# Performance work log

Measured on AMD Instinct MI355X. Metric: run time of the kernel, lower is better.

Reference implementation:

```python
import jax, jax.numpy as jnp
import numpy as np

B, S, D = 8, 2048, 256


def setup_inputs() -> dict:
    key = jax.random.key(0)
    kq, kk, kv, km = jax.random.split(key, 4)
    q = jax.random.normal(kq, (B, S, D), dtype=jnp.float32)
    k = jax.random.normal(kk, (B, S, D), dtype=jnp.float32)
    v = jax.random.normal(kv, (B, S, D), dtype=jnp.float32)
    mask = jax.random.randint(km, (B, S, S), 0, 2, dtype=jnp.int32)
    return {"q": q, "k": k, "v": v, "mask": mask}


def reference(q, k, v, mask):
    d_k = q.shape[-1]
    scale = 1.0 / jnp.sqrt(jnp.float32(d_k))
    # scores: [B, S, S]
    attn = jnp.einsum('bqd,bkd->bqk', q, k) * scale
    attn = jnp.where(mask == 0, jnp.float32(-1e9), attn)
    attn = jax.nn.softmax(attn, axis=-1)
    out = jnp.einsum('bqk,bkd->bqd', attn, v)
    return (out, attn)
```

## Files before the change

kernel.cpp:

```cpp
#include <hip/hip_runtime.h>

constexpr int B = 8, S = 2048, D = 256;
constexpr int TQ = 32;
constexpr float SCALE = 0.0625f;
constexpr int PSTRIDE = 2056;

typedef __attribute__((ext_vector_type(8))) short bf16x8;
typedef __attribute__((ext_vector_type(4))) float f32x4;

__device__ __forceinline__ short f2bf(float f) {
    union { float f; unsigned u; } c; c.f = f;
    unsigned u = c.u + 0x7fffu + ((c.u >> 16) & 1u);
    return (short)(u >> 16);
}

__global__ void conv_bf16(const float* __restrict__ in, short* __restrict__ out, int n4) {
    int i = blockIdx.x * blockDim.x + threadIdx.x;
    if (i < n4) {
        float4 v = ((const float4*)in)[i];
        short4 o; o.x = f2bf(v.x); o.y = f2bf(v.y); o.z = f2bf(v.z); o.w = f2bf(v.w);
        ((short4*)out)[i] = o;
    }
}

__global__ void transpose_v(const float* __restrict__ v, short* __restrict__ vt) {
    const int b = blockIdx.z;
    const int d0 = blockIdx.x * 64, k0 = blockIdx.y * 64;
    const int t = threadIdx.x;
    const int tr = t >> 4, tc = t & 15;
    __shared__ float tile[64][65];
    const float* vb = v + (size_t)b * S * D;
    #pragma unroll
    for (int r = 0; r < 4; ++r) {
        int key = r * 16 + tr;
        float4 x = *(const float4*)(vb + (size_t)(k0 + key) * D + d0 + tc * 4);
        tile[key][tc * 4 + 0] = x.x; tile[key][tc * 4 + 1] = x.y;
        tile[key][tc * 4 + 2] = x.z; tile[key][tc * 4 + 3] = x.w;
    }
    __syncthreads();
    short* vtb = vt + (size_t)b * D * S;
    #pragma unroll
    for (int r = 0; r < 4; ++r) {
        int d = r * 16 + tr;
        short4 o;
        o.x = f2bf(tile[tc * 4 + 0][d]); o.y = f2bf(tile[tc * 4 + 1][d]);
        o.z = f2bf(tile[tc * 4 + 2][d]); o.w = f2bf(tile[tc * 4 + 3][d]);
        *(short4*)(vtb + (size_t)(d0 + d) * S + k0 + tc * 4) = o;
    }
}

__global__ __launch_bounds__(512, 2) void attn_mfma(
    const short* __restrict__ qb, const short* __restrict__ kb,
    const short* __restrict__ vtb, const int* __restrict__ maskg,
    float* __restrict__ outg, float* __restrict__ attng)
{
    const int b = blockIdx.y;
    const int i0 = blockIdx.x * TQ;
    const int tid = threadIdx.x;
    const int wave = tid >> 6, lane = tid & 63;
    const int quad = lane >> 4, l16 = lane & 15;

    __shared__ short p_lds[TQ][PSTRIDE];
    __shared__ float red[8][TQ];

    bf16x8 aq[2][8];
    const short* qbase = qb + ((size_t)b * S + i0) * D;
    #pragma unroll
    for (int mt = 0; mt < 2; ++mt)
        #pragma unroll
        for (int ks = 0; ks < 8; ++ks)
            aq[mt][ks] = *(const bf16x8*)(qbase + (size_t)(mt * 16 + l16) * D + ks * 32 + quad * 8);

    f32x4 acc[2][16];
    #pragma unroll
    for (int mt = 0; mt < 2; ++mt)
        #pragma unroll
        for (int nt = 0; nt < 16; ++nt)
            acc[mt][nt] = f32x4{0.f, 0.f, 0.f, 0.f};

    const short* kbase = kb + (size_t)b * S * D;
    #pragma unroll
    for (int nt = 0; nt < 16; ++nt) {
        const int n0 = wave * 256 + nt * 16;
        bf16x8 bk[8];
        #pragma unroll
        for (int ks = 0; ks < 8; ++ks)
            bk[ks] = *(const bf16x8*)(kbase + (size_t)(n0 + l16) * D + ks * 32 + quad * 8);
        #pragma unroll
        for (int ks = 0; ks < 8; ++ks) {
            acc[0][nt] = __builtin_amdgcn_mfma_f32_16x16x32_bf16(aq[0][ks], bk[ks], acc[0][nt], 0, 0, 0);
            acc[1][nt] = __builtin_amdgcn_mfma_f32_16x16x32_bf16(aq[1][ks], bk[ks], acc[1][nt], 0, 0, 0);
        }
    }

    float rsum[2][4];
    #pragma unroll
    for (int mt = 0; mt < 2; ++mt)
        #pragma unroll
        for (int r = 0; r < 4; ++r) rsum[mt][r] = 0.f;

    #pragma unroll
    for (int mt = 0; mt < 2; ++mt) {
        const int* mbase = maskg + ((size_t)b * S + i0 + mt * 16 + quad * 4) * S;
        #pragma unroll
        for (int nt = 0; nt < 16; ++nt) {
            const int col = wave * 256 + nt * 16 + l16;
            #pragma unroll
            for (int r = 0; r < 4; ++r) {
                int m = mbase[(size_t)r * S + col];
                float s = (m == 0) ? -1e9f : acc[mt][nt][r] * SCALE;
                float e = __expf(s);
                acc[mt][nt][r] = e;
                rsum[mt][r] += e;
            }
        }
    }
    #pragma unroll
    for (int mt = 0; mt < 2; ++mt)
        #pragma unroll
        for (int r = 0; r < 4; ++r) {
            float v = rsum[mt][r];
            v += __shfl_xor(v, 1); v += __shfl_xor(v, 2);
            v += __shfl_xor(v, 4); v += __shfl_xor(v, 8);
            rsum[mt][r] = v;
            if (l16 == 0) red[wave][mt * 16 + quad * 4 + r] = v;
        }
    __syncthreads();

    float inv[2][4];
    #pragma unroll
    for (int mt = 0; mt < 2; ++mt)
        #pragma unroll
        for (int r = 0; r < 4; ++r) {
            float tot = 0.f;
            #pragma unroll
            for (int w = 0; w < 8; ++w) tot += red[w][mt * 16 + quad * 4 + r];
            inv[mt][r] = 1.0f / tot;
        }

    #pragma unroll
    for (int mt = 0; mt < 2; ++mt) {
        float* abase = attng + ((size_t)b * S + i0 + mt * 16 + quad * 4) * S;
        #pragma unroll
        for (int nt = 0; nt < 16; ++nt) {
            const int col = wave * 256 + nt * 16 + l16;
            #pragma unroll
            for (int r = 0; r < 4; ++r) {
                float p = acc[mt][nt][r] * inv[mt][r];
                abase[(size_t)r * S + col] = p;
                p_lds[mt * 16 + quad * 4 + r][col] = f2bf(p);
            }
        }
    }
    __syncthreads();

    f32x4 oacc[2][2];
    #pragma unroll
    for (int mt = 0; mt < 2; ++mt)
        #pragma unroll
        for (int nc = 0; nc < 2; ++nc) oacc[mt][nc] = f32x4{0.f, 0.f, 0.f, 0.f};

    const short* vbase = vtb + (size_t)b * D * S;
    const int nb = wave * 32;
    for (int ks = 0; ks < 64; ++ks) {
        bf16x8 ap[2], bv[2];
        #pragma unroll
        for (int mt = 0; mt < 2; ++mt)
            ap[mt] = *(const bf16x8*)&p_lds[mt * 16 + l16][ks * 32 + quad * 8];
        #pragma unroll
        for (int nc = 0; nc < 2; ++nc)
            bv[nc] = *(const bf16x8*)(vbase + (size_t)(nb + nc * 16 + l16) * S + ks * 32 + quad * 8);
        #pragma unroll
        for (int mt = 0; mt < 2; ++mt)
            #pragma unroll
            for (int nc = 0; nc < 2; ++nc)
                oacc[mt][nc] = __builtin_amdgcn_mfma_f32_16x16x32_bf16(ap[mt], bv[nc], oacc[mt][nc], 0, 0, 0);
    }

    #pragma unroll
    for (int mt = 0; mt < 2; ++mt)
        #pragma unroll
        for (int nc = 0; nc < 2; ++nc)
            #pragma unroll
            for (int r = 0; r < 4; ++r) {
                int row = i0 + mt * 16 + quad * 4 + r;
                int col = nb + nc * 16 + l16;
                outg[((size_t)b * S + row) * D + col] = oacc[mt][nc][r];
            }
}

extern "C" void kernel_launch(void* const* d_in, const int* in_sizes, int n_in,
                              void* d_out, int out_size, void* d_ws, size_t ws_size,
                              hipStream_t stream) {
    const float* q    = (const float*)d_in[0];
    const float* k    = (const float*)d_in[1];
    const float* v    = (const float*)d_in[2];
    const int*   mask = (const int*)d_in[3];
    float* out  = (float*)d_out;
    float* attn = out + (size_t)B * S * D;

    const size_t N = (size_t)B * S * D;
    short* qb  = (short*)d_ws;
    short* kb  = qb + N;
    short* vtb = kb + N;

    const int n4 = (int)(N / 4);
    conv_bf16<<<dim3(n4 / 256), 256, 0, stream>>>(q, qb, n4);
    conv_bf16<<<dim3(n4 / 256), 256, 0, stream>>>(k, kb, n4);
    transpose_v<<<dim3(D / 64, S / 64, B), 256, 0, stream>>>(v, vtb);

    attn_mfma<<<dim3(S / TQ, B), 512, 0, stream>>>(qb, kb, vtb, mask, out, attn);
}
```

Measured before the change: 412.2 us.

## Halve query tile to 16 rows for higher occupancy, use nontemporal mask/attn loads/stores

```diff
diff --git a/kernel.cpp b/kernel.cpp
--- a/kernel.cpp
+++ b/kernel.cpp
@@ -1,7 +1,7 @@
 #include <hip/hip_runtime.h>
 
 constexpr int B = 8, S = 2048, D = 256;
-constexpr int TQ = 32;
+constexpr int TQ = 16;
 constexpr float SCALE = 0.0625f;
 constexpr int PSTRIDE = 2056;
 
@@ -49,7 +49,7 @@
     }
 }
 
-__global__ __launch_bounds__(512, 2) void attn_mfma(
+__global__ __launch_bounds__(512, 4) void attn_mfma(
     const short* __restrict__ qb, const short* __restrict__ kb,
     const short* __restrict__ vtb, const int* __restrict__ maskg,
     float* __restrict__ outg, float* __restrict__ attng)
@@ -63,20 +63,16 @@
     __shared__ short p_lds[TQ][PSTRIDE];
     __shared__ float red[8][TQ];
 
-    bf16x8 aq[2][8];
+    bf16x8 aq[8];
     const short* qbase = qb + ((size_t)b * S + i0) * D;
     #pragma unroll
-    for (int mt = 0; mt < 2; ++mt)
-        #pragma unroll
-        for (int ks = 0; ks < 8; ++ks)
-            aq[mt][ks] = *(const bf16x8*)(qbase + (size_t)(mt * 16 + l16) * D + ks * 32 + quad * 8);
+    for (int ks = 0; ks < 8; ++ks)
+        aq[ks] = *(const bf16x8*)(qbase + (size_t)l16 * D + ks * 32 + quad * 8);
 
-    f32x4 acc[2][16];
+    f32x4 acc[16];
     #pragma unroll
-    for (int mt = 0; mt < 2; ++mt)
-        #pragma unroll
-        for (int nt = 0; nt < 16; ++nt)
-            acc[mt][nt] = f32x4{0.f, 0.f, 0.f, 0.f};
+    for (int nt = 0; nt < 16; ++nt)
+        acc[nt] = f32x4{0.f, 0.f, 0.f, 0.f};
 
     const short* kbase = kb + (size_t)b * S * D;
     #pragma unroll
@@ -87,106 +83,88 @@
         for (int ks = 0; ks < 8; ++ks)
             bk[ks] = *(const bf16x8*)(kbase + (size_t)(n0 + l16) * D + ks * 32 + quad * 8);
         #pragma unroll
-        for (int ks = 0; ks < 8; ++ks) {
-            acc[0][nt] = __builtin_amdgcn_mfma_f32_16x16x32_bf16(aq[0][ks], bk[ks], acc[0][nt], 0, 0, 0);
-            acc[1][nt] = __builtin_amdgcn_mfma_f32_16x16x32_bf16(aq[1][ks], bk[ks], acc[1][nt], 0, 0, 0);
-        }
+        for (int ks = 0; ks < 8; ++ks)
+            acc[nt] = __builtin_amdgcn_mfma_f32_16x16x32_bf16(aq[ks], bk[ks], acc[nt], 0, 0, 0);
     }
 
-    float rsum[2][4];
+    float rsum[4];
     #pragma unroll
-    for (int mt = 0; mt < 2; ++mt)
-        #pragma unroll
-        for (int r = 0; r < 4; ++r) rsum[mt][r] = 0.f;
+    for (int r = 0; r < 4; ++r) rsum[r] = 0.f;
 
-    #pragma unroll
-    for (int mt = 0; mt < 2; ++mt) {
-        const int* mbase = maskg + ((size_t)b * S + i0 + mt * 16 + quad * 4) * S;
+    {
+        const int* mbase = maskg + ((size_t)b * S + i0 + quad * 4) * S;
         #pragma unroll
         for (int nt = 0; nt < 16; ++nt) {
             const int col = wave * 256 + nt * 16 + l16;
             #pragma unroll
             for (int r = 0; r < 4; ++r) {
-                int m = mbase[(size_t)r * S + col];
-                float s = (m == 0) ? -1e9f : acc[mt][nt][r] * SCALE;
+                int m = __builtin_nontemporal_load(mbase + (size_t)r * S + col);
+                float s = (m == 0) ? -1e9f : acc[nt][r] * SCALE;
                 float e = __expf(s);
-                acc[mt][nt][r] = e;
-                rsum[mt][r] += e;
+                acc[nt][r] = e;
+                rsum[r] += e;
             }
         }
     }
     #pragma unroll
-    for (int mt = 0; mt < 2; ++mt)
-        #pragma unroll
-        for (int r = 0; r < 4; ++r) {
-            float v = rsum[mt][r];
-            v += __shfl_xor(v, 1); v += __shfl_xor(v, 2);
-            v += __shfl_xor(v, 4); v += __shfl_xor(v, 8);
-            rsum[mt][r] = v;
-            if (l16 == 0) red[wave][mt * 16 + quad * 4 + r] = v;
-        }
+    for (int r = 0; r < 4; ++r) {
+        float v = rsum[r];
+        v += __shfl_xor(v, 1); v += __shfl_xor(v, 2);
+        v += __shfl_xor(v, 4); v += __shfl_xor(v, 8);
+        rsum[r] = v;
+        if (l16 == 0) red[wave][quad * 4 + r] = v;
+    }
     __syncthreads();
 
-    float inv[2][4];
+    float inv[4];
     #pragma unroll
-    for (int mt = 0; mt < 2; ++mt)
+    for (int r = 0; r < 4; ++r) {
+        float tot = 0.f;
         #pragma unroll
-        for (int r = 0; r < 4; ++r) {
-            float tot = 0.f;
-            #pragma unroll
-            for (int w = 0; w < 8; ++w) tot += red[w][mt * 16 + quad * 4 + r];
-            inv[mt][r] = 1.0f / tot;
-        }
+        for (int w = 0; w < 8; ++w) tot += red[w][quad * 4 + r];
+        inv[r] = 1.0f / tot;
+    }
 
-    #pragma unroll
-    for (int mt = 0; mt < 2; ++mt) {
-        float* abase = attng + ((size_t)b * S + i0 + mt * 16 + quad * 4) * S;
+    {
+        float* abase = attng + ((size_t)b * S + i0 + quad * 4) * S;
         #pragma unroll
         for (int nt = 0; nt < 16; ++nt) {
             const int col = wave * 256 + nt * 16 + l16;
             #pragma unroll
             for (int r = 0; r < 4; ++r) {
-                float p = acc[mt][nt][r] * inv[mt][r];
-                abase[(size_t)r * S + col] = p;
-                p_lds[mt * 16 + quad * 4 + r][col] = f2bf(p);
+                float p = acc[nt][r] * inv[r];
+                __builtin_nontemporal_store(p, abase + (size_t)r * S + col);
+                p_lds[quad * 4 + r][col] = f2bf(p);
             }
         }
     }
     __syncthreads();
 
-    f32x4 oacc[2][2];
+    f32x4 oacc[2];
     #pragma unroll
-    for (int mt = 0; mt < 2; ++mt)
-        #pragma unroll
-        for (int nc = 0; nc < 2; ++nc) oacc[mt][nc] = f32x4{0.f, 0.f, 0.f, 0.f};
+    for (int nc = 0; nc < 2; ++nc) oacc[nc] = f32x4{0.f, 0.f, 0.f, 0.f};
 
     const short* vbase = vtb + (size_t)b * D * S;
     const int nb = wave * 32;
     for (int ks = 0; ks < 64; ++ks) {
-        bf16x8 ap[2], bv[2];
-        #pragma unroll
-        for (int mt = 0; mt < 2; ++mt)
-            ap[mt] = *(const bf16x8*)&p_lds[mt * 16 + l16][ks * 32 + quad * 8];
+        bf16x8 ap, bv[2];
+        ap = *(const bf16x8*)&p_lds[l16][ks * 32 + quad * 8];
         #pragma unroll
         for (int nc = 0; nc < 2; ++nc)
             bv[nc] = *(const bf16x8*)(vbase + (size_t)(nb + nc * 16 + l16) * S + ks * 32 + quad * 8);
         #pragma unroll
-        for (int mt = 0; mt < 2; ++mt)
-            #pragma unroll
-            for (int nc = 0; nc < 2; ++nc)
-                oacc[mt][nc] = __builtin_amdgcn_mfma_f32_16x16x32_bf16(ap[mt], bv[nc], oacc[mt][nc], 0, 0, 0);
+        for (int nc = 0; nc < 2; ++nc)
+            oacc[nc] = __builtin_amdgcn_mfma_f32_16x16x32_bf16(ap, bv[nc], oacc[nc], 0, 0, 0);
     }
 
     #pragma unroll
-    for (int mt = 0; mt < 2; ++mt)
+    for (int nc = 0; nc < 2; ++nc)
         #pragma unroll
-        for (int nc = 0; nc < 2; ++nc)
-            #pragma unroll
-            for (int r = 0; r < 4; ++r) {
-                int row = i0 + mt * 16 + quad * 4 + r;
-                int col = nb + nc * 16 + l16;
-                outg[((size_t)b * S + row) * D + col] = oacc[mt][nc][r];
-            }
+        for (int r = 0; r < 4; ++r) {
+            int row = i0 + quad * 4 + r;
+            int col = nb + nc * 16 + l16;
+            __builtin_nontemporal_store(oacc[nc][r], outg + ((size_t)b * S + row) * D + col);
+        }
 }
 
 extern "C" void kernel_launch(void* const* d_in, const int* in_sizes, int n_in,
```

Result: slower. 540.2 us (+31.1%).
